# Kernel optimization log

Measured on AMD Instinct MI355X. Metric: run time of the kernel, lower is better.

## Reference

```python
import jax, jax.numpy as jnp
import numpy as np

H = 256
W = 256
ALPHA_THRESH = 1.0 / 255.0


def _project(xyz, cholesky):
    # means in (-1,1) -> pixel coords; cholesky lower-tri L=[[l1,0],[l2,l3]] (+bound)
    means = jnp.tanh(xyz)                              # [N,2]
    chol = cholesky + jnp.array([0.5, 0.0, 0.5], dtype=cholesky.dtype)
    cx = 0.5 * W * (means[:, 0] + 1.0)                 # [N]
    cy = 0.5 * H * (means[:, 1] + 1.0)
    l1, l2, l3 = chol[:, 0], chol[:, 1], chol[:, 2]
    # cov = L L^T = [[l1^2, l1*l2],[l1*l2, l2^2+l3^2]]
    a = l1 * l1
    b = l1 * l2
    c = l2 * l2 + l3 * l3
    det = a * c - b * b
    conic_a = c / det
    conic_b = -b / det
    conic_c = a / det
    return cx, cy, conic_a, conic_b, conic_c


def _render(xyz, cholesky, features, opacity):
    cx, cy, ca, cb, cc = _project(xyz, cholesky)
    # pixel centers
    px = jnp.arange(W, dtype=jnp.float32) + 0.5        # [W]
    py = jnp.arange(H, dtype=jnp.float32) + 0.5        # [H]
    pxs = jnp.tile(px, H)                              # [HW]
    pys = jnp.repeat(py, W)                            # [HW]
    dx = cx[:, None] - pxs[None, :]                    # [N,HW]
    dy = cy[:, None] - pys[None, :]
    sigma = 0.5 * (ca[:, None] * dx * dx + cc[:, None] * dy * dy) + cb[:, None] * dx * dy
    alpha = jnp.minimum(0.999, opacity * jnp.exp(-sigma))  # [N,HW]
    valid = (sigma >= 0.0) & (alpha >= ALPHA_THRESH)
    w = jnp.where(valid, alpha, 0.0)
    out = jnp.einsum('np,nc->pc', w, features)         # accumulated-sum rasterization
    out = jnp.clip(out, 0.0, 1.0)
    out = out.reshape(1, H, W, 3).transpose(0, 3, 1, 2)  # [1,3,H,W]
    return out


def setup_inputs() -> dict:
    key = jax.random.key(0)
    k1, k2, k3 = jax.random.split(key, 3)
    N = 1024
    u = jax.random.uniform(k1, (N, 2), dtype=jnp.float32, minval=0.001, maxval=0.999)
    _xyz = jnp.arctanh(2.0 * (u - 0.5))
    _cholesky = jax.random.uniform(k2, (N, 3), dtype=jnp.float32)
    _features_dc = jax.random.uniform(k3, (N, 3), dtype=jnp.float32)
    _opacity = jnp.ones((N, 1), dtype=jnp.float32)
    return {"_xyz": _xyz, "_cholesky": _cholesky, "_features_dc": _features_dc, "_opacity": _opacity}


def reference(_xyz, _cholesky, _features_dc, _opacity):
    return _render(_xyz, _cholesky, _features_dc, _opacity)
```

## Files before the change

kernel.cpp:

```cpp
#include <hip/hip_runtime.h>
#include <math.h>


constexpr int HH = 256;
constexpr int WW = 256;
constexpr int TILE = 16;
constexpr int MAXG = 1024;
constexpr float ALPHA_T = 1.0f / 255.0f;

__global__ __launch_bounds__(256) void gsplat_render(
    const float* __restrict__ xyz,
    const float* __restrict__ chol,
    const float* __restrict__ feat,
    const float* __restrict__ opac,
    float* __restrict__ out,
    int N)
{
    __shared__ float4 cA[MAXG];
    __shared__ float4 cB[MAXG];
    __shared__ float  cC[MAXG];
    __shared__ int    s_cnt;

    const int tid = threadIdx.x;
    if (tid == 0) s_cnt = 0;
    __syncthreads();

    const int tx = blockIdx.x & 15;
    const int ty = blockIdx.x >> 4;
    const float x0c = (float)(tx * TILE) + 0.5f;
    const float x1c = (float)(tx * TILE + TILE - 1) + 0.5f;
    const float y0c = (float)(ty * TILE) + 0.5f;
    const float y1c = (float)(ty * TILE + TILE - 1) + 0.5f;

    for (int i = tid; i < N; i += 256) {
        float mx = tanhf(xyz[2 * i]);
        float my = tanhf(xyz[2 * i + 1]);
        float cx = 0.5f * (float)WW * (mx + 1.0f);
        float cy = 0.5f * (float)HH * (my + 1.0f);
        float l1 = chol[3 * i]     + 0.5f;
        float l2 = chol[3 * i + 1];
        float l3 = chol[3 * i + 2] + 0.5f;
        float a = l1 * l1;
        float b = l1 * l2;
        float c = l2 * l2 + l3 * l3;
        float det = a * c - b * b;
        float ca = c / det;
        float cb = -b / det;
        float cc = a / det;
        float op = opac[i];

        float T   = __logf(255.0f * op);
        float s2T = sqrtf(2.0f * T);
        float rx  = s2T * l1 + 0.05f;
        float ry  = s2T * sqrtf(c) + 0.05f;

        bool hit = (cx + rx >= x0c) && (cx - rx <= x1c) &&
                   (cy + ry >= y0c) && (cy - ry <= y1c);
        if (hit) {
            int slot = atomicAdd(&s_cnt, 1);
            if (slot < MAXG) {
                cA[slot] = make_float4(cx, cy, ca, cb);
                cB[slot] = make_float4(cc, op, feat[3 * i], feat[3 * i + 1]);
                cC[slot] = feat[3 * i + 2];
            }
        }
    }
    __syncthreads();
    const int cnt = min(s_cnt, MAXG);

    const int lx = tid & 15;
    const int ly = tid >> 4;
    const int x = tx * TILE + lx;
    const int y = ty * TILE + ly;
    const float px = (float)x + 0.5f;
    const float py = (float)y + 0.5f;

    float accr = 0.0f, accg = 0.0f, accb = 0.0f;
    for (int j = 0; j < cnt; ++j) {
        float4 A = cA[j];
        float4 B = cB[j];
        float fb = cC[j];
        float dx = A.x - px;
        float dy = A.y - py;
        float sigma = 0.5f * (A.z * dx * dx + B.x * dy * dy) + A.w * dx * dy;
        float alpha = fminf(0.999f, B.y * __expf(-sigma));
        float w = (sigma >= 0.0f && alpha >= ALPHA_T) ? alpha : 0.0f;
        accr = fmaf(w, B.z, accr);
        accg = fmaf(w, B.w, accg);
        accb = fmaf(w, fb, accb);
    }

    const int p = y * WW + x;
    out[p]                 = fminf(fmaxf(accr, 0.0f), 1.0f);
    out[HH * WW + p]       = fminf(fmaxf(accg, 0.0f), 1.0f);
    out[2 * HH * WW + p]   = fminf(fmaxf(accb, 0.0f), 1.0f);
}

extern "C" void kernel_launch(void* const* d_in, const int* in_sizes, int n_in,
                              void* d_out, int out_size, void* d_ws, size_t ws_size,
                              hipStream_t stream) {
    const float* xyz  = (const float*)d_in[0];
    const float* chol = (const float*)d_in[1];
    const float* feat = (const float*)d_in[2];
    const float* opac = (const float*)d_in[3];
    float* out = (float*)d_out;
    const int N = in_sizes[0] / 2;

    gsplat_render<<<dim3(256), dim3(256), 0, stream>>>(xyz, chol, feat, opac, out, N);
}
```

Measured before the change: 64.11 us.

## Project gaussians once and bin into per-tile lists before rendering

Splits the renderer into a single-block projection kernel that computes each gaussian's parameters once and scatters its index into per-tile lists via global atomics, and a render kernel that gathers only its tile's gaussians into shared memory. This removes the redundant per-block projection of all gaussians. It adds a second launch, global atomics, and a workspace round trip, and the serial single-block first stage may limit parallelism.

```diff
diff --git a/kernel.cpp b/kernel.cpp
--- a/kernel.cpp
+++ b/kernel.cpp
@@ -5,34 +5,27 @@
 constexpr int HH = 256;
 constexpr int WW = 256;
 constexpr int TILE = 16;
+constexpr int NT = 16;
 constexpr int MAXG = 1024;
 constexpr float ALPHA_T = 1.0f / 255.0f;
 
-__global__ __launch_bounds__(256) void gsplat_render(
+__global__ __launch_bounds__(1024) void k1_project_scatter(
     const float* __restrict__ xyz,
     const float* __restrict__ chol,
     const float* __restrict__ feat,
     const float* __restrict__ opac,
-    float* __restrict__ out,
+    float4* __restrict__ P0,
+    float4* __restrict__ P1,
+    float*  __restrict__ Pb,
+    int* __restrict__ counters,
+    int* __restrict__ lists,
     int N)
 {
-    __shared__ float4 cA[MAXG];
-    __shared__ float4 cB[MAXG];
-    __shared__ float  cC[MAXG];
-    __shared__ int    s_cnt;
-
     const int tid = threadIdx.x;
-    if (tid == 0) s_cnt = 0;
+    if (tid < NT * NT) counters[tid] = 0;
     __syncthreads();
 
-    const int tx = blockIdx.x & 15;
-    const int ty = blockIdx.x >> 4;
-    const float x0c = (float)(tx * TILE) + 0.5f;
-    const float x1c = (float)(tx * TILE + TILE - 1) + 0.5f;
-    const float y0c = (float)(ty * TILE) + 0.5f;
-    const float y1c = (float)(ty * TILE + TILE - 1) + 0.5f;
-
-    for (int i = tid; i < N; i += 256) {
+    for (int i = tid; i < N; i += 1024) {
         float mx = tanhf(xyz[2 * i]);
         float my = tanhf(xyz[2 * i + 1]);
         float cx = 0.5f * (float)WW * (mx + 1.0f);
@@ -49,37 +42,67 @@
         float cc = a / det;
         float op = opac[i];
 
+        P0[i] = make_float4(cx, cy, ca, cb);
+        P1[i] = make_float4(cc, op, feat[3 * i], feat[3 * i + 1]);
+        Pb[i] = feat[3 * i + 2];
+
         float T   = __logf(255.0f * op);
         float s2T = sqrtf(2.0f * T);
         float rx  = s2T * l1 + 0.05f;
         float ry  = s2T * sqrtf(c) + 0.05f;
 
-        bool hit = (cx + rx >= x0c) && (cx - rx <= x1c) &&
-                   (cy + ry >= y0c) && (cy - ry <= y1c);
-        if (hit) {
-            int slot = atomicAdd(&s_cnt, 1);
-            if (slot < MAXG) {
-                cA[slot] = make_float4(cx, cy, ca, cb);
-                cB[slot] = make_float4(cc, op, feat[3 * i], feat[3 * i + 1]);
-                cC[slot] = feat[3 * i + 2];
+        bool ok = (cx == cx) && (cy == cy) && (rx == rx) && (ry == ry);
+        if (!ok) continue;
+
+        int tx0 = max(0,      (int)ceilf ((cx - rx - 15.5f) * (1.0f / 16.0f)));
+        int tx1 = min(NT - 1, (int)floorf((cx + rx - 0.5f)  * (1.0f / 16.0f)));
+        int ty0 = max(0,      (int)ceilf ((cy - ry - 15.5f) * (1.0f / 16.0f)));
+        int ty1 = min(NT - 1, (int)floorf((cy + ry - 0.5f)  * (1.0f / 16.0f)));
+        for (int ty = ty0; ty <= ty1; ++ty)
+            for (int tx = tx0; tx <= tx1; ++tx) {
+                int t = ty * NT + tx;
+                int slot = atomicAdd(&counters[t], 1);
+                lists[t * MAXG + slot] = i;
             }
-        }
+    }
+}
+
+__global__ __launch_bounds__(256) void k2_render(
+    const float4* __restrict__ P0,
+    const float4* __restrict__ P1,
+    const float*  __restrict__ Pb,
+    const int* __restrict__ counters,
+    const int* __restrict__ lists,
+    float* __restrict__ out)
+{
+    __shared__ float4 sA[MAXG];
+    __shared__ float4 sB[MAXG];
+    __shared__ float  sC[MAXG];
+
+    const int tile = blockIdx.x;
+    const int tid = threadIdx.x;
+    const int cnt = counters[tile];
+
+    for (int j = tid; j < cnt; j += 256) {
+        int idx = lists[tile * MAXG + j];
+        sA[j] = P0[idx];
+        sB[j] = P1[idx];
+        sC[j] = Pb[idx];
     }
     __syncthreads();
-    const int cnt = min(s_cnt, MAXG);
 
-    const int lx = tid & 15;
-    const int ly = tid >> 4;
-    const int x = tx * TILE + lx;
-    const int y = ty * TILE + ly;
+    const int tx = tile & (NT - 1);
+    const int ty = tile >> 4;
+    const int x = tx * TILE + (tid & 15);
+    const int y = ty * TILE + (tid >> 4);
     const float px = (float)x + 0.5f;
     const float py = (float)y + 0.5f;
 
     float accr = 0.0f, accg = 0.0f, accb = 0.0f;
     for (int j = 0; j < cnt; ++j) {
-        float4 A = cA[j];
-        float4 B = cB[j];
-        float fb = cC[j];
+        float4 A = sA[j];
+        float4 B = sB[j];
+        float fb = sC[j];
         float dx = A.x - px;
         float dy = A.y - py;
         float sigma = 0.5f * (A.z * dx * dx + B.x * dy * dy) + A.w * dx * dy;
@@ -91,9 +114,9 @@
     }
 
     const int p = y * WW + x;
-    out[p]                 = fminf(fmaxf(accr, 0.0f), 1.0f);
-    out[HH * WW + p]       = fminf(fmaxf(accg, 0.0f), 1.0f);
-    out[2 * HH * WW + p]   = fminf(fmaxf(accb, 0.0f), 1.0f);
+    out[p]               = fminf(fmaxf(accr, 0.0f), 1.0f);
+    out[HH * WW + p]     = fminf(fmaxf(accg, 0.0f), 1.0f);
+    out[2 * HH * WW + p] = fminf(fmaxf(accb, 0.0f), 1.0f);
 }
 
 extern "C" void kernel_launch(void* const* d_in, const int* in_sizes, int n_in,
@@ -106,5 +129,15 @@
     float* out = (float*)d_out;
     const int N = in_sizes[0] / 2;
 
-    gsplat_render<<<dim3(256), dim3(256), 0, stream>>>(xyz, chol, feat, opac, out, N);
+    char* ws = (char*)d_ws;
+    int*    counters = (int*)ws;
+    int*    lists    = (int*)(ws + 1024);
+    float4* P0       = (float4*)(ws + 1024 + 256 * MAXG * 4);
+    float4* P1       = P0 + MAXG;
+    float*  Pb       = (float*)(P1 + MAXG);
+
+    k1_project_scatter<<<dim3(1), dim3(1024), 0, stream>>>(
+        xyz, chol, feat, opac, P0, P1, Pb, counters, lists, N);
+    k2_render<<<dim3(256), dim3(256), 0, stream>>>(
+        P0, P1, Pb, counters, lists, out);
 }
```

After: 66.25 us. 3.3% more time.
